# Kernel tuning notes

Hardware: AMD Instinct MI355X
Metric: run time of the kernel (lower is better)

## Reference

```python
import jax, jax.numpy as jnp
import numpy as np

D = 1024
H = 16
HD = D // H


def setup_inputs() -> dict:
    key = jax.random.key(0)
    ks = jax.random.split(key, 13)
    s = 0.02
    inp = {
        "x": jax.random.normal(ks[0], (2, 2048, D), dtype=jnp.float32),
        "Wq": jax.random.normal(ks[1], (D, D), dtype=jnp.float32) * s,
        "bq": jnp.zeros((D,), jnp.float32),
        "Wk": jax.random.normal(ks[2], (D, D), dtype=jnp.float32) * s,
        "bk": jnp.zeros((D,), jnp.float32),
        "Wv": jax.random.normal(ks[3], (D, D), dtype=jnp.float32) * s,
        "bv": jnp.zeros((D,), jnp.float32),
        "Wo": jax.random.normal(ks[4], (D, D), dtype=jnp.float32) * s,
        "bo": jnp.zeros((D,), jnp.float32),
        "W1": jax.random.normal(ks[5], (D, 4 * D), dtype=jnp.float32) * s,
        "b1": jnp.zeros((4 * D,), jnp.float32),
        "W2": jax.random.normal(ks[6], (4 * D, D), dtype=jnp.float32) * s,
        "b2": jnp.zeros((D,), jnp.float32),
    }
    return inp


def reference(x, Wq, bq, Wk, bk, Wv, bv, Wo, bo, W1, b1, W2, b2):
    B, L, _ = x.shape
    # attention (dropout = identity in eval); note: original forward never applies norm1/norm2
    q = (x @ Wq + bq).reshape(B, L, H, HD).transpose(0, 2, 1, 3)  # [B,H,L,HD]
    k = (x @ Wk + bk).reshape(B, L, H, HD).transpose(0, 2, 1, 3)
    v = (x @ Wv + bv).reshape(B, L, H, HD).transpose(0, 2, 1, 3)
    s = jnp.einsum("bhqd,bhkd->bhqk", q, k) / jnp.sqrt(jnp.float32(HD))
    causal = jnp.tril(jnp.ones((L, L), dtype=bool))
    s = jnp.where(causal[None, None, :, :], s, -jnp.inf)
    p = jax.nn.softmax(s, axis=-1)
    y = jnp.einsum("bhqk,bhkd->bhqd", p, v)
    y = y.transpose(0, 2, 1, 3).reshape(B, L, D)
    x = x + (y @ Wo + bo)
    # MLP with SiLU
    h = jax.nn.silu(x @ W1 + b1)
    x = x + (h @ W2 + b2)
    return x
```

## Files before the change

kernel.cpp:

```cpp
#include <hip/hip_runtime.h>
#include <hip/hip_bf16.h>
#include <stdint.h>

using u16 = unsigned short;
typedef __bf16 bf16x8 __attribute__((ext_vector_type(8)));
typedef float f32x4 __attribute__((ext_vector_type(4)));
typedef u16 u16x8 __attribute__((ext_vector_type(8)));

__device__ __forceinline__ float bf2f(u16 u) {
  union { unsigned int i; float f; } v; v.i = ((unsigned int)u) << 16; return v.f;
}
__device__ __forceinline__ u16 f2bf(float f) {
  __bf16 h = (__bf16)f;
  return __builtin_bit_cast(u16, h);
}
__device__ __forceinline__ float fexp2(float x) {
  return __builtin_amdgcn_exp2f(x);
}

__device__ __forceinline__ void gload_lds16(const void* g, void* l) {
  __builtin_amdgcn_global_load_lds(
      (__attribute__((address_space(1))) const void*)g,
      (__attribute__((address_space(3))) void*)l, 16, 0, 0);
}

__global__ void cvt_f32_bf16(const float* __restrict__ in, u16* __restrict__ out) {
  int i = (blockIdx.x * 256 + threadIdx.x) * 8;
  float4 a = *(const float4*)(in + i);
  float4 b = *(const float4*)(in + i + 4);
  u16x8 o;
  o[0] = f2bf(a.x); o[1] = f2bf(a.y); o[2] = f2bf(a.z); o[3] = f2bf(a.w);
  o[4] = f2bf(b.x); o[5] = f2bf(b.y); o[6] = f2bf(b.z); o[7] = f2bf(b.w);
  *(u16x8*)(out + i) = o;
}

__global__ void transpose_cvt(const float* __restrict__ W, u16* __restrict__ Wt,
                              int K, int N) {
  __shared__ float t[32][33];
  const int tx = threadIdx.x & 31, ty = threadIdx.x >> 5;
  const int n0 = blockIdx.x * 32, k0 = blockIdx.y * 32;
#pragma unroll
  for (int i = 0; i < 32; i += 8)
    t[ty + i][tx] = W[(size_t)(k0 + ty + i) * N + n0 + tx];
  __syncthreads();
#pragma unroll
  for (int i = 0; i < 32; i += 8)
    Wt[(size_t)(n0 + ty + i) * K + k0 + tx] = f2bf(t[tx][ty + i]);
}

__global__ void transpose_cvt4(const float* __restrict__ Wa, const float* __restrict__ Wb,
                               const float* __restrict__ Wc, const float* __restrict__ Wd,
                               u16* __restrict__ Da, u16* __restrict__ Db,
                               u16* __restrict__ Dc, u16* __restrict__ Dd) {
  __shared__ float t[32][33];
  const int z = blockIdx.z;
  const float* W = (z == 0) ? Wa : (z == 1) ? Wb : (z == 2) ? Wc : Wd;
  u16* D = (z == 0) ? Da : (z == 1) ? Db : (z == 2) ? Dc : Dd;
  const int tx = threadIdx.x & 31, ty = threadIdx.x >> 5;
  const int n0 = blockIdx.x * 32, k0 = blockIdx.y * 32;
#pragma unroll
  for (int i = 0; i < 32; i += 8)
    t[ty + i][tx] = W[(size_t)(k0 + ty + i) * 1024 + n0 + tx];
  __syncthreads();
#pragma unroll
  for (int i = 0; i < 32; i += 8)
    D[(size_t)(n0 + ty + i) * 1024 + k0 + tx] = f2bf(t[tx][ty + i]);
}

__global__ void transpose_v(const u16* __restrict__ qkv, u16* __restrict__ vt) {
  __shared__ u16 tile[32][34];
  const int tx = threadIdx.x & 31, ty = threadIdx.x >> 5;
  const int kv0 = blockIdx.x * 32, d0 = blockIdx.y * 32;
  const int bh = blockIdx.z, b = bh >> 4, h = bh & 15;
#pragma unroll
  for (int i = 0; i < 32; i += 8)
    tile[ty + i][tx] = qkv[(size_t)(b * 2048 + kv0 + ty + i) * 3072 + 2048 + h * 64 + d0 + tx];
  __syncthreads();
#pragma unroll
  for (int i = 0; i < 32; i += 8)
    vt[((size_t)bh * 64 + d0 + ty + i) * 2048 + kv0 + tx] = tile[tx][ty + i];
}

__global__ void concat_bias(const float* __restrict__ bq, const float* __restrict__ bk,
                            const float* __restrict__ bv, float* __restrict__ o) {
  int i = blockIdx.x * 256 + threadIdx.x;
  o[i] = (i < 1024) ? bq[i] : (i < 2048 ? bk[i - 1024] : bv[i - 2048]);
}

template <int EPI>
__global__ __launch_bounds__(512, 2) void gemm256_kernel(
    const u16* __restrict__ A, const u16* __restrict__ Bt,
    const float* __restrict__ bias, u16* __restrict__ outb,
    int M, int N, int K) {
  __shared__ u16 As[4][8192];
  __shared__ u16 Bs[4][8192];
  const int t = threadIdx.x;
  const int w = t >> 6, lane = t & 63, lr = lane & 15, lg = lane >> 4;
  const int wm = w >> 2, wn = w & 3;
  const int gx = gridDim.x;
  const int nwg = gx * gridDim.y;
  const int p = blockIdx.y * gx + blockIdx.x;
  const int L = (p & 7) * (nwg >> 3) + (p >> 3);
  const int m0 = (L / gx) * 256, n0 = (L % gx) * 256;

  f32x4 acc[8][4] = {};
  bf16x8 bfr[4];
  const int NKT = K >> 5;

  auto stageA = [&](int kt) {
#pragma unroll
    for (int l = 0; l < 2; ++l) {
      int slot = l * 512 + t;
      int row = slot >> 2, cs = slot & 3;
      gload_lds16(&A[(size_t)(m0 + row) * K + kt * 32 + cs * 8], &As[kt & 3][slot * 8]);
    }
  };
  auto stageB = [&](int kt) {
#pragma unroll
    for (int l = 0; l < 2; ++l) {
      int slot = l * 512 + t;
      int row = slot >> 2, cs = slot & 3;
      gload_lds16(&Bt[(size_t)(n0 + row) * K + kt * 32 + cs * 8], &Bs[kt & 3][slot * 8]);
    }
  };

  stageA(0); stageB(0); stageA(1); stageB(1); stageA(2); stageB(2);
  asm volatile("s_waitcnt vmcnt(8)" ::: "memory");
  __builtin_amdgcn_s_barrier();

#define PHASE(Q, STAGE)                                                          \
  {                                                                              \
    const u16* Ab = &As[kt & 3][0];                                              \
    bf16x8 af[4];                                                                \
    _Pragma("unroll") for (int m = 0; m < 4; ++m)                                \
        af[m] = *(const bf16x8*)&Ab[(wm * 128 + ((Q) * 4 + m) * 16 + lr) * 32 +  \
                                    lg * 8];                                     \
    if ((Q) == 0) {                                                              \
      const u16* Bb = &Bs[kt & 3][0];                                            \
      _Pragma("unroll") for (int n = 0; n < 4; ++n)                              \
          bfr[n] = *(const bf16x8*)&Bb[(wn * 64 + n * 16 + lr) * 32 + lg * 8];   \
    }                                                                            \
    STAGE;                                                                       \
    __builtin_amdgcn_s_barrier();                                                \
    asm volatile("s_waitcnt lgkmcnt(0)" ::: "memory");                           \
    __builtin_amdgcn_sched_barrier(0);                                           \
    __builtin_amdgcn_s_setprio(1);                                               \
    _Pragma("unroll") for (int m = 0; m < 4; ++m)                                \
        _Pragma("unroll") for (int n = 0; n < 4; ++n)                            \
            acc[(Q) * 4 + m][n] = __builtin_amdgcn_mfma_f32_16x16x32_bf16(       \
                af[m], bfr[n], acc[(Q) * 4 + m][n], 0, 0, 0);                    \
    __builtin_amdgcn_s_setprio(0);                                               \
  }

  int kt = 0;
  for (; kt < NKT - 3; ++kt) {
    PHASE(0, stageA(kt + 3));
    __builtin_amdgcn_s_barrier();
    PHASE(1, stageB(kt + 3));
    asm volatile("s_waitcnt vmcnt(8)" ::: "memory");
    __builtin_amdgcn_s_barrier();
  }
  asm volatile("s_waitcnt vmcnt(0)" ::: "memory");
  __builtin_amdgcn_s_barrier();
  for (; kt < NKT; ++kt) {
    PHASE(0, (void)0);
    __builtin_amdgcn_s_barrier();
    PHASE(1, (void)0);
    __builtin_amdgcn_s_barrier();
  }
#undef PHASE

#pragma unroll
  for (int mf = 0; mf < 8; ++mf)
#pragma unroll
    for (int nf = 0; nf < 4; ++nf)
#pragma unroll
      for (int i = 0; i < 4; ++i) {
        int gr = m0 + wm * 128 + mf * 16 + lg * 4 + i;
        int gc = n0 + wn * 64 + nf * 16 + lr;
        float v = acc[mf][nf][i] + bias[gc];
        if constexpr (EPI == 1) v = v / (1.f + __expf(-v));
        outb[(size_t)gr * N + gc] = f2bf(v);
      }
}

template <int EPI>
__global__ __launch_bounds__(256) void gemm_nk64_kernel(
    const u16* __restrict__ A, const u16* __restrict__ Bt,
    const float* __restrict__ bias, const float* __restrict__ resid,
    u16* __restrict__ outb, float* __restrict__ outf, int M, int N, int K) {
  __shared__ u16 As[2][128 * 64];
  __shared__ u16 Bs[2][64 * 64];
  const int t = threadIdx.x;
  const int w = t >> 6, lane = t & 63, lr = lane & 15, lg = lane >> 4;
  const int wm = w >> 1, wn = w & 1;
  const int gx = gridDim.x;
  const int nwg = gx * gridDim.y;
  const int p = blockIdx.y * gx + blockIdx.x;
  const int L = (p & 7) * (nwg >> 3) + (p >> 3);
  const int m0 = (L / gx) * 128, n0 = (L % gx) * 64;

  f32x4 acc[4][2] = {};
  const int nt = K >> 6;

  auto stage = [&](int kt, int buf) {
#pragma unroll
    for (int it = 0; it < 4; ++it) {
      int ofs = (it * 256 + t) * 8;
      int row = ofs >> 6, slot = (ofs >> 3) & 7, ss = slot ^ (row & 7);
      gload_lds16(&A[(size_t)(m0 + row) * K + kt * 64 + ss * 8], &As[buf][ofs]);
    }
#pragma unroll
    for (int it = 0; it < 2; ++it) {
      int ofs = (it * 256 + t) * 8;
      int row = ofs >> 6, slot = (ofs >> 3) & 7, ss = slot ^ (row & 7);
      gload_lds16(&Bt[(size_t)(n0 + row) * K + kt * 64 + ss * 8], &Bs[buf][ofs]);
    }
  };

  stage(0, 0);
  __syncthreads();

  for (int kt = 0; kt < nt; ++kt) {
    const int cur = kt & 1;
    if (kt + 1 < nt) stage(kt + 1, cur ^ 1);
#pragma unroll
    for (int kk = 0; kk < 64; kk += 32) {
      const int kcol = kk + lg * 8;
      bf16x8 af[4], bfr[2];
#pragma unroll
      for (int m = 0; m < 4; ++m) {
        int row = wm * 64 + m * 16 + lr;
        int ss = (kcol >> 3) ^ (row & 7);
        af[m] = *(const bf16x8*)&As[cur][row * 64 + ss * 8];
      }
#pragma unroll
      for (int n = 0; n < 2; ++n) {
        int row = wn * 32 + n * 16 + lr;
        int ss = (kcol >> 3) ^ (row & 7);
        bfr[n] = *(const bf16x8*)&Bs[cur][row * 64 + ss * 8];
      }
#pragma unroll
      for (int m = 0; m < 4; ++m)
#pragma unroll
        for (int n = 0; n < 2; ++n)
          acc[m][n] = __builtin_amdgcn_mfma_f32_16x16x32_bf16(af[m], bfr[n],
                                                              acc[m][n], 0, 0, 0);
    }
    __syncthreads();
  }

  const int r0 = m0 + wm * 64, c0 = n0 + wn * 32;
#pragma unroll
  for (int m = 0; m < 4; ++m)
#pragma unroll
    for (int n = 0; n < 2; ++n)
#pragma unroll
      for (int i = 0; i < 4; ++i) {
        int gr = r0 + m * 16 + lg * 4 + i;
        int gc = c0 + n * 16 + lr;
        float v = acc[m][n][i] + bias[gc];
        if constexpr (EPI == 2 || EPI == 3) v += resid[(size_t)gr * N + gc];
        if constexpr (EPI == 2) {
          outf[(size_t)gr * N + gc] = v;
          outb[(size_t)gr * N + gc] = f2bf(v);
        }
        if constexpr (EPI == 3) outf[(size_t)gr * N + gc] = v;
      }
}

__global__ __launch_bounds__(256) void attn_kernel(const u16* __restrict__ qkv,
                                                   const u16* __restrict__ vtg,
                                                   u16* __restrict__ out) {
  __shared__ u16 Ks[2][64 * 64];
  __shared__ u16 Vs[2][64 * 64];
  __shared__ u16 Ps[4][32 * 64];
  const int t = threadIdx.x, w = t >> 6, lane = t & 63, lr = lane & 15, lg = lane >> 4;
  const int p = blockIdx.y * 16 + blockIdx.x;
  const int L = (p & 7) * 64 + (p >> 3);
  const int qt = 15 - (L & 15), bh = L >> 4, b = bh >> 4, h = bh & 15;
  const int qbw = qt * 128 + w * 32;
  const int jmax_blk = 2 * qt + 1;
  const int jmax_w = 2 * qt + (w >> 1);

  const float QS = 0.18033688011f;
  bf16x8 qf[2][2];
#pragma unroll
  for (int m = 0; m < 2; ++m)
#pragma unroll
    for (int kc = 0; kc < 2; ++kc) {
      const u16x8 v = *(const u16x8*)&qkv[(size_t)(b * 2048 + qbw + m * 16 + lr) * 3072 +
                                          h * 64 + kc * 32 + lg * 8];
      bf16x8 q;
#pragma unroll
      for (int jj = 0; jj < 8; ++jj) q[jj] = (__bf16)(bf2f(v[jj]) * QS);
      qf[m][kc] = q;
    }

  f32x4 yacc[2][4] = {};
  float S[2] = {0.f, 0.f};

  auto stage = [&](int j, int buf) {
#pragma unroll
    for (int it = 0; it < 2; ++it) {
      int ofs = (it * 256 + t) * 8;
      int row = ofs >> 6, slot = (ofs >> 3) & 7, ss = slot ^ (row & 7);
      gload_lds16(&qkv[(size_t)(b * 2048 + j * 64 + row) * 3072 + 1024 + h * 64 + ss * 8],
                  &Ks[buf][ofs]);
      gload_lds16(&vtg[((size_t)bh * 64 + row) * 2048 + j * 64 + ss * 8],
                  &Vs[buf][ofs]);
    }
  };

  stage(0, 0);
  __syncthreads();

  for (int j = 0; j <= jmax_blk; ++j) {
    const int cur = j & 1;
    if (j < jmax_blk) stage(j + 1, cur ^ 1);

    if (j <= jmax_w) {
      bf16x8 kf[2][4];
#pragma unroll
      for (int kc = 0; kc < 2; ++kc)
#pragma unroll
        for (int n = 0; n < 4; ++n) {
          int row = n * 16 + lr;
          kf[kc][n] = *(const bf16x8*)((const char*)&Ks[cur][0] + row * 128 +
                                       ((kc * 64 + lg * 16) ^ ((row & 7) << 4)));
        }
      f32x4 s[2][4] = {};
#pragma unroll
      for (int m = 0; m < 2; ++m)
#pragma unroll
        for (int n = 0; n < 4; ++n)
#pragma unroll
          for (int kc = 0; kc < 2; ++kc)
            s[m][n] = __builtin_amdgcn_mfma_f32_16x16x32_bf16(kf[kc][n], qf[m][kc],
                                                              s[m][n], 0, 0, 0);
      if (j * 64 + 63 > qbw) {
#pragma unroll
        for (int m = 0; m < 2; ++m)
#pragma unroll
          for (int n = 0; n < 4; ++n)
#pragma unroll
            for (int i = 0; i < 4; ++i) {
              int kabs = j * 64 + n * 16 + lg * 4 + i;
              int qabs = qbw + m * 16 + lr;
              if (kabs > qabs) s[m][n][i] = -1e30f;
            }
      }
#pragma unroll
      for (int m = 0; m < 2; ++m) {
        float rs = 0.f;
#pragma unroll
        for (int n = 0; n < 4; ++n)
#pragma unroll
          for (int i = 0; i < 4; ++i) {
            float pv = fexp2(s[m][n][i]);
            s[m][n][i] = pv;
            rs += pv;
          }
        S[m] += rs;
        const int qrow = m * 16 + lr, sw = (qrow & 7) << 4;
#pragma unroll
        for (int n = 0; n < 4; ++n) {
          ushort4 ph;
          ph.x = f2bf(s[m][n][0]); ph.y = f2bf(s[m][n][1]);
          ph.z = f2bf(s[m][n][2]); ph.w = f2bf(s[m][n][3]);
          *(ushort4*)((char*)&Ps[w][0] + qrow * 128 + ((n * 32 + lg * 8) ^ sw)) = ph;
        }
      }
#pragma unroll
      for (int kc = 0; kc < 2; ++kc) {
        bf16x8 pa[2], vtf[4];
#pragma unroll
        for (int m = 0; m < 2; ++m) {
          int qrow = m * 16 + lr;
          pa[m] = *(const bf16x8*)((const char*)&Ps[w][0] + qrow * 128 +
                                   ((kc * 64 + lg * 16) ^ ((qrow & 7) << 4)));
        }
#pragma unroll
        for (int n = 0; n < 4; ++n) {
          int row = n * 16 + lr;
          vtf[n] = *(const bf16x8*)((const char*)&Vs[cur][0] + row * 128 +
                                    ((kc * 64 + lg * 16) ^ ((row & 7) << 4)));
        }
#pragma unroll
        for (int m = 0; m < 2; ++m)
#pragma unroll
          for (int n = 0; n < 4; ++n)
            yacc[m][n] = __builtin_amdgcn_mfma_f32_16x16x32_bf16(pa[m], vtf[n],
                                                                 yacc[m][n], 0, 0, 0);
      }
    }
    __syncthreads();
  }

#pragma unroll
  for (int m = 0; m < 2; ++m) {
    float Sv = S[m];
    Sv += __shfl_xor(Sv, 16, 64);
    Sv += __shfl_xor(Sv, 32, 64);
    float inv = 1.f / Sv;
#pragma unroll
    for (int i = 0; i < 4; ++i) {
      float ivq = __shfl(inv, lg * 4 + i, 64);
#pragma unroll
      for (int n = 0; n < 4; ++n) {
        int row = b * 2048 + qbw + m * 16 + lg * 4 + i;
        int col = h * 64 + n * 16 + lr;
        out[(size_t)row * 1024 + col] = f2bf(yacc[m][n][i] * ivq);
      }
    }
  }
}

extern "C" void kernel_launch(void* const* d_in, const int* in_sizes, int n_in,
                              void* d_out, int out_size, void* d_ws, size_t ws_size,
                              hipStream_t stream) {
  const float* x  = (const float*)d_in[0];
  const float* Wq = (const float*)d_in[1];
  const float* bq = (const float*)d_in[2];
  const float* Wk = (const float*)d_in[3];
  const float* bk = (const float*)d_in[4];
  const float* Wv = (const float*)d_in[5];
  const float* bv = (const float*)d_in[6];
  const float* Wo = (const float*)d_in[7];
  const float* bo = (const float*)d_in[8];
  const float* W1 = (const float*)d_in[9];
  const float* b1 = (const float*)d_in[10];
  const float* W2 = (const float*)d_in[11];
  const float* b2 = (const float*)d_in[12];
  float* out = (float*)d_out;

  char* ws = (char*)d_ws;
  const size_t MB = 1u << 20;
  u16*   xb    = (u16*)(ws + 0);
  u16*   wtqkv = (u16*)(ws + 8 * MB);
  u16*   wto   = (u16*)(ws + 14 * MB);
  u16*   wt1   = (u16*)(ws + 16 * MB);
  u16*   wt2   = (u16*)(ws + 24 * MB);
  float* bqkv  = (float*)(ws + 32 * MB);
  u16*   qkv   = (u16*)(ws + 33 * MB);
  u16*   attn  = (u16*)(ws + 57 * MB);
  float* x2f   = (float*)(ws + 65 * MB);
  u16*   x2b   = (u16*)(ws + 81 * MB);
  u16*   hbuf  = (u16*)(ws + 89 * MB);
  u16*   vtg   = xb;

  cvt_f32_bf16<<<2048, 256, 0, stream>>>(x, xb);
  transpose_cvt4<<<dim3(32, 32, 4), 256, 0, stream>>>(
      Wq, Wk, Wv, Wo, wtqkv, wtqkv + 1024 * 1024, wtqkv + 2 * 1024 * 1024, wto);
  transpose_cvt<<<dim3(128, 32), 256, 0, stream>>>(W1, wt1, 1024, 4096);
  transpose_cvt<<<dim3(32, 128), 256, 0, stream>>>(W2, wt2, 4096, 1024);
  concat_bias<<<12, 256, 0, stream>>>(bq, bk, bv, bqkv);

  gemm256_kernel<0><<<dim3(12, 16), 512, 0, stream>>>(
      xb, wtqkv, bqkv, qkv, 4096, 3072, 1024);
  transpose_v<<<dim3(64, 2, 32), 256, 0, stream>>>(qkv, vtg);
  attn_kernel<<<dim3(16, 32), 256, 0, stream>>>(qkv, vtg, attn);
  gemm_nk64_kernel<2><<<dim3(16, 32), 256, 0, stream>>>(
      attn, wto, bo, x, x2b, x2f, 4096, 1024, 1024);
  gemm256_kernel<1><<<dim3(16, 16), 512, 0, stream>>>(
      x2b, wt1, b1, hbuf, 4096, 4096, 1024);
  gemm_nk64_kernel<3><<<dim3(16, 32), 256, 0, stream>>>(
      hbuf, wt2, b2, x2f, nullptr, out, 4096, 1024, 4096);
}
```

Baseline: 234.5 us.

## Replace W2 GEMM with two-pass split-K kernel using 128x128 tiles

The final MLP down-projection (K=4096) moves from the 128x64-tile kernel to a new 128x128-tile kernel. K is split into two halves run as two sequential launches: the first writes fp32 partial sums to a scratch buffer (reusing the qkv region), and the second adds partials, bias and residual. The larger tile raises operand reuse per workgroup but halves the grid to 256 blocks per pass. In exchange it adds a second launch and a full fp32 partial round-trip through memory, and the passes do not run concurrently.

```diff
diff --git a/kernel.cpp b/kernel.cpp
--- a/kernel.cpp
+++ b/kernel.cpp
@@ -260,12 +260,94 @@
         int gr = r0 + m * 16 + lg * 4 + i;
         int gc = c0 + n * 16 + lr;
         float v = acc[m][n][i] + bias[gc];
-        if constexpr (EPI == 2 || EPI == 3) v += resid[(size_t)gr * N + gc];
         if constexpr (EPI == 2) {
+          v += resid[(size_t)gr * N + gc];
           outf[(size_t)gr * N + gc] = v;
           outb[(size_t)gr * N + gc] = f2bf(v);
         }
-        if constexpr (EPI == 3) outf[(size_t)gr * N + gc] = v;
+      }
+}
+
+template <int PASS>
+__global__ __launch_bounds__(256) void gemm_splitk_kernel(
+    const u16* __restrict__ A, const u16* __restrict__ Bt,
+    const float* __restrict__ bias, const float* __restrict__ resid,
+    float* __restrict__ partial, float* __restrict__ outf,
+    int M, int N, int K) {
+  __shared__ u16 As[2][128 * 64];
+  __shared__ u16 Bs[2][128 * 64];
+  const int t = threadIdx.x;
+  const int w = t >> 6, lane = t & 63, lr = lane & 15, lg = lane >> 4;
+  const int wm = w >> 1, wn = w & 1;
+  const int gx = gridDim.x;
+  const int nwg = gx * gridDim.y;
+  const int p = blockIdx.y * gx + blockIdx.x;
+  const int L = (p & 7) * (nwg >> 3) + (p >> 3);
+  const int m0 = (L / gx) * 128, n0 = (L % gx) * 128;
+  const int KH = K >> 1;
+  const int kbase = PASS * KH;
+
+  f32x4 acc[4][4] = {};
+  const int nt = KH >> 6;
+
+  auto stage = [&](int kt, int buf) {
+#pragma unroll
+    for (int it = 0; it < 4; ++it) {
+      int ofs = (it * 256 + t) * 8;
+      int row = ofs >> 6, slot = (ofs >> 3) & 7, ss = slot ^ (row & 7);
+      gload_lds16(&A[(size_t)(m0 + row) * K + kbase + kt * 64 + ss * 8], &As[buf][ofs]);
+      gload_lds16(&Bt[(size_t)(n0 + row) * K + kbase + kt * 64 + ss * 8], &Bs[buf][ofs]);
+    }
+  };
+
+  stage(0, 0);
+  __syncthreads();
+
+  for (int kt = 0; kt < nt; ++kt) {
+    const int cur = kt & 1;
+    if (kt + 1 < nt) stage(kt + 1, cur ^ 1);
+#pragma unroll
+    for (int kk = 0; kk < 64; kk += 32) {
+      const int kcol = kk + lg * 8;
+      bf16x8 af[4], bfr[4];
+#pragma unroll
+      for (int m = 0; m < 4; ++m) {
+        int row = wm * 64 + m * 16 + lr;
+        int ss = (kcol >> 3) ^ (row & 7);
+        af[m] = *(const bf16x8*)&As[cur][row * 64 + ss * 8];
+      }
+#pragma unroll
+      for (int n = 0; n < 4; ++n) {
+        int row = wn * 64 + n * 16 + lr;
+        int ss = (kcol >> 3) ^ (row & 7);
+        bfr[n] = *(const bf16x8*)&Bs[cur][row * 64 + ss * 8];
+      }
+#pragma unroll
+      for (int m = 0; m < 4; ++m)
+#pragma unroll
+        for (int n = 0; n < 4; ++n)
+          acc[m][n] = __builtin_amdgcn_mfma_f32_16x16x32_bf16(af[m], bfr[n],
+                                                              acc[m][n], 0, 0, 0);
+    }
+    __syncthreads();
+  }
+
+  const int r0 = m0 + wm * 64, c0 = n0 + wn * 64;
+#pragma unroll
+  for (int m = 0; m < 4; ++m)
+#pragma unroll
+    for (int n = 0; n < 4; ++n)
+#pragma unroll
+      for (int i = 0; i < 4; ++i) {
+        int gr = r0 + m * 16 + lg * 4 + i;
+        int gc = c0 + n * 16 + lr;
+        if constexpr (PASS == 0) {
+          partial[(size_t)gr * N + gc] = acc[m][n][i];
+        } else {
+          float v = acc[m][n][i] + partial[(size_t)gr * N + gc] + bias[gc] +
+                    resid[(size_t)gr * N + gc];
+          outf[(size_t)gr * N + gc] = v;
+        }
       }
 }
 
@@ -448,6 +530,7 @@
   u16*   x2b   = (u16*)(ws + 81 * MB);
   u16*   hbuf  = (u16*)(ws + 89 * MB);
   u16*   vtg   = xb;
+  float* partial = (float*)(ws + 33 * MB);
 
   cvt_f32_bf16<<<2048, 256, 0, stream>>>(x, xb);
   transpose_cvt4<<<dim3(32, 32, 4), 256, 0, stream>>>(
@@ -464,6 +547,8 @@
       attn, wto, bo, x, x2b, x2f, 4096, 1024, 1024);
   gemm256_kernel<1><<<dim3(16, 16), 512, 0, stream>>>(
       x2b, wt1, b1, hbuf, 4096, 4096, 1024);
-  gemm_nk64_kernel<3><<<dim3(16, 32), 256, 0, stream>>>(
-      hbuf, wt2, b2, x2f, nullptr, out, 4096, 1024, 4096);
-}
+  gemm_splitk_kernel<0><<<dim3(8, 32), 256, 0, stream>>>(
+      hbuf, wt2, nullptr, nullptr, partial, nullptr, 4096, 1024, 4096);
+  gemm_splitk_kernel<1><<<dim3(8, 32), 256, 0, stream>>>(
+      hbuf, wt2, b2, x2f, partial, out, 4096, 1024, 4096);
+}
```

Measured after the change: 254.7 us. 8.6% more time.

## Shrink attention query tile to 64 rows per block and double grid

Applied to the files above, without the earlier changes.

Each attention block now covers 64 query rows, with each wave owning 16 rows instead of 32, and the grid doubles to 1024 blocks. The causal loop runs over exactly qt+1 key tiles, the per-wave skip logic is gone, and masking applies only on the diagonal tile. This cuts per-wave register state and causal load imbalance, and makes more blocks available for the CUs. In exchange, each K/V tile staged into LDS feeds half as many queries, so global K/V traffic roughly doubles, and the K fragments are reused across only one MFMA row-tile.

```diff
diff --git a/kernel.cpp b/kernel.cpp
--- a/kernel.cpp
+++ b/kernel.cpp
@@ -274,31 +274,27 @@
                                                    u16* __restrict__ out) {
   __shared__ u16 Ks[2][64 * 64];
   __shared__ u16 Vs[2][64 * 64];
-  __shared__ u16 Ps[4][32 * 64];
+  __shared__ u16 Ps[4][16 * 64];
   const int t = threadIdx.x, w = t >> 6, lane = t & 63, lr = lane & 15, lg = lane >> 4;
-  const int p = blockIdx.y * 16 + blockIdx.x;
-  const int L = (p & 7) * 64 + (p >> 3);
-  const int qt = 15 - (L & 15), bh = L >> 4, b = bh >> 4, h = bh & 15;
-  const int qbw = qt * 128 + w * 32;
-  const int jmax_blk = 2 * qt + 1;
-  const int jmax_w = 2 * qt + (w >> 1);
+  const int p = blockIdx.y * 32 + blockIdx.x;
+  const int L = (p & 7) * 128 + (p >> 3);
+  const int qt = 31 - (L & 31), bh = L >> 5, b = bh >> 4, h = bh & 15;
+  const int qbw = qt * 64 + w * 16;
 
   const float QS = 0.18033688011f;
-  bf16x8 qf[2][2];
-#pragma unroll
-  for (int m = 0; m < 2; ++m)
-#pragma unroll
-    for (int kc = 0; kc < 2; ++kc) {
-      const u16x8 v = *(const u16x8*)&qkv[(size_t)(b * 2048 + qbw + m * 16 + lr) * 3072 +
-                                          h * 64 + kc * 32 + lg * 8];
-      bf16x8 q;
-#pragma unroll
-      for (int jj = 0; jj < 8; ++jj) q[jj] = (__bf16)(bf2f(v[jj]) * QS);
-      qf[m][kc] = q;
-    }
-
-  f32x4 yacc[2][4] = {};
-  float S[2] = {0.f, 0.f};
+  bf16x8 qf[2];
+#pragma unroll
+  for (int kc = 0; kc < 2; ++kc) {
+    const u16x8 v = *(const u16x8*)&qkv[(size_t)(b * 2048 + qbw + lr) * 3072 +
+                                        h * 64 + kc * 32 + lg * 8];
+    bf16x8 q;
+#pragma unroll
+    for (int jj = 0; jj < 8; ++jj) q[jj] = (__bf16)(bf2f(v[jj]) * QS);
+    qf[kc] = q;
+  }
+
+  f32x4 yacc[4] = {};
+  float S = 0.f;
 
   auto stage = [&](int j, int buf) {
 #pragma unroll
@@ -315,91 +311,80 @@
   stage(0, 0);
   __syncthreads();
 
-  for (int j = 0; j <= jmax_blk; ++j) {
+  for (int j = 0; j <= qt; ++j) {
     const int cur = j & 1;
-    if (j < jmax_blk) stage(j + 1, cur ^ 1);
-
-    if (j <= jmax_w) {
-      bf16x8 kf[2][4];
+    if (j < qt) stage(j + 1, cur ^ 1);
+
+    bf16x8 kf[2][4];
+#pragma unroll
+    for (int kc = 0; kc < 2; ++kc)
+#pragma unroll
+      for (int n = 0; n < 4; ++n) {
+        int row = n * 16 + lr;
+        kf[kc][n] = *(const bf16x8*)((const char*)&Ks[cur][0] + row * 128 +
+                                     ((kc * 64 + lg * 16) ^ ((row & 7) << 4)));
+      }
+    f32x4 s[4] = {};
+#pragma unroll
+    for (int n = 0; n < 4; ++n)
 #pragma unroll
       for (int kc = 0; kc < 2; ++kc)
-#pragma unroll
-        for (int n = 0; n < 4; ++n) {
-          int row = n * 16 + lr;
-          kf[kc][n] = *(const bf16x8*)((const char*)&Ks[cur][0] + row * 128 +
-                                       ((kc * 64 + lg * 16) ^ ((row & 7) << 4)));
+        s[n] = __builtin_amdgcn_mfma_f32_16x16x32_bf16(kf[kc][n], qf[kc],
+                                                       s[n], 0, 0, 0);
+    if (j == qt) {
+#pragma unroll
+      for (int n = 0; n < 4; ++n)
+#pragma unroll
+        for (int i = 0; i < 4; ++i) {
+          int kabs = j * 64 + n * 16 + lg * 4 + i;
+          int qabs = qbw + lr;
+          if (kabs > qabs) s[n][i] = -1e30f;
         }
-      f32x4 s[2][4] = {};
-#pragma unroll
-      for (int m = 0; m < 2; ++m)
-#pragma unroll
-        for (int n = 0; n < 4; ++n)
-#pragma unroll
-          for (int kc = 0; kc < 2; ++kc)
-            s[m][n] = __builtin_amdgcn_mfma_f32_16x16x32_bf16(kf[kc][n], qf[m][kc],
-                                                              s[m][n], 0, 0, 0);
-      if (j * 64 + 63 > qbw) {
-#pragma unroll
-        for (int m = 0; m < 2; ++m)
-#pragma unroll
-          for (int n = 0; n < 4; ++n)
-#pragma unroll
-            for (int i = 0; i < 4; ++i) {
-              int kabs = j * 64 + n * 16 + lg * 4 + i;
-              int qabs = qbw + m * 16 + lr;
-              if (kabs > qabs) s[m][n][i] = -1e30f;
-            }
-      }
-#pragma unroll
-      for (int m = 0; m < 2; ++m) {
-        float rs = 0.f;
-#pragma unroll
-        for (int n = 0; n < 4; ++n)
-#pragma unroll
-          for (int i = 0; i < 4; ++i) {
-            float pv = fexp2(s[m][n][i]);
-            s[m][n][i] = pv;
-            rs += pv;
-          }
-        S[m] += rs;
-        const int qrow = m * 16 + lr, sw = (qrow & 7) << 4;
-#pragma unroll
-        for (int n = 0; n < 4; ++n) {
-          ushort4 ph;
-          ph.x = f2bf(s[m][n][0]); ph.y = f2bf(s[m][n][1]);
-          ph.z = f2bf(s[m][n][2]); ph.w = f2bf(s[m][n][3]);
-          *(ushort4*)((char*)&Ps[w][0] + qrow * 128 + ((n * 32 + lg * 8) ^ sw)) = ph;
+    }
+    {
+      float rs = 0.f;
+#pragma unroll
+      for (int n = 0; n < 4; ++n)
+#pragma unroll
+        for (int i = 0; i < 4; ++i) {
+          float pv = fexp2(s[n][i]);
+          s[n][i] = pv;
+          rs += pv;
         }
-      }
-#pragma unroll
-      for (int kc = 0; kc < 2; ++kc) {
-        bf16x8 pa[2], vtf[4];
-#pragma unroll
-        for (int m = 0; m < 2; ++m) {
-          int qrow = m * 16 + lr;
-          pa[m] = *(const bf16x8*)((const char*)&Ps[w][0] + qrow * 128 +
-                                   ((kc * 64 + lg * 16) ^ ((qrow & 7) << 4)));
-        }
-#pragma unroll
-        for (int n = 0; n < 4; ++n) {
-          int row = n * 16 + lr;
-          vtf[n] = *(const bf16x8*)((const char*)&Vs[cur][0] + row * 128 +
-                                    ((kc * 64 + lg * 16) ^ ((row & 7) << 4)));
-        }
-#pragma unroll
-        for (int m = 0; m < 2; ++m)
-#pragma unroll
-          for (int n = 0; n < 4; ++n)
-            yacc[m][n] = __builtin_amdgcn_mfma_f32_16x16x32_bf16(pa[m], vtf[n],
-                                                                 yacc[m][n], 0, 0, 0);
-      }
+      S += rs;
+      const int qrow = lr, sw = (qrow & 7) << 4;
+#pragma unroll
+      for (int n = 0; n < 4; ++n) {
+        ushort4 ph;
+        ph.x = f2bf(s[n][0]); ph.y = f2bf(s[n][1]);
+        ph.z = f2bf(s[n][2]); ph.w = f2bf(s[n][3]);
+        *(ushort4*)((char*)&Ps[w][0] + qrow * 128 + ((n * 32 + lg * 8) ^ sw)) = ph;
+      }
+    }
+#pragma unroll
+    for (int kc = 0; kc < 2; ++kc) {
+      bf16x8 pa, vtf[4];
+      {
+        int qrow = lr;
+        pa = *(const bf16x8*)((const char*)&Ps[w][0] + qrow * 128 +
+                              ((kc * 64 + lg * 16) ^ ((qrow & 7) << 4)));
+      }
+#pragma unroll
+      for (int n = 0; n < 4; ++n) {
+        int row = n * 16 + lr;
+        vtf[n] = *(const bf16x8*)((const char*)&Vs[cur][0] + row * 128 +
+                                  ((kc * 64 + lg * 16) ^ ((row & 7) << 4)));
+      }
+#pragma unroll
+      for (int n = 0; n < 4; ++n)
+        yacc[n] = __builtin_amdgcn_mfma_f32_16x16x32_bf16(pa, vtf[n],
+                                                          yacc[n], 0, 0, 0);
     }
     __syncthreads();
   }
 
-#pragma unroll
-  for (int m = 0; m < 2; ++m) {
-    float Sv = S[m];
+  {
+    float Sv = S;
     Sv += __shfl_xor(Sv, 16, 64);
     Sv += __shfl_xor(Sv, 32, 64);
     float inv = 1.f / Sv;
@@ -408,9 +393,9 @@
       float ivq = __shfl(inv, lg * 4 + i, 64);
 #pragma unroll
       for (int n = 0; n < 4; ++n) {
-        int row = b * 2048 + qbw + m * 16 + lg * 4 + i;
+        int row = b * 2048 + qbw + lg * 4 + i;
         int col = h * 64 + n * 16 + lr;
-        out[(size_t)row * 1024 + col] = f2bf(yacc[m][n][i] * ivq);
+        out[(size_t)row * 1024 + col] = f2bf(yacc[n][i] * ivq);
       }
     }
   }
@@ -459,7 +444,7 @@
   gemm256_kernel<0><<<dim3(12, 16), 512, 0, stream>>>(
       xb, wtqkv, bqkv, qkv, 4096, 3072, 1024);
   transpose_v<<<dim3(64, 2, 32), 256, 0, stream>>>(qkv, vtg);
-  attn_kernel<<<dim3(16, 32), 256, 0, stream>>>(qkv, vtg, attn);
+  attn_kernel<<<dim3(32, 32), 256, 0, stream>>>(qkv, vtg, attn);
   gemm_nk64_kernel<2><<<dim3(16, 32), 256, 0, stream>>>(
       attn, wto, bo, x, x2b, x2f, 4096, 1024, 1024);
   gemm256_kernel<1><<<dim3(16, 16), 512, 0, stream>>>(
```

Measured after the change: 236.3 us. No clear change (+0.8%).
